# Performance work log

Hardware: AMD Instinct MI355X
Metric: run time of the kernel (lower is better)

Reference implementation:

```python
import jax, jax.numpy as jnp
import numpy as np

EMBED_DIM = 768
NUM_HEADS = 12
HEAD_DIM = EMBED_DIM // NUM_HEADS  # 64
SCALE = HEAD_DIM ** -0.5
B, S = 32, 512


def setup_inputs() -> dict:
    key = jax.random.key(0)
    ks = jax.random.split(key, 10)
    std = EMBED_DIM ** -0.5
    hidden_states = jax.random.normal(ks[0], (B, S, EMBED_DIM), dtype=jnp.float32)
    # causal mask: 0 on/below diagonal, large negative above
    neg = jnp.full((S, S), -1e9, dtype=jnp.float32)
    causal_attention_mask = jnp.broadcast_to(
        jnp.triu(neg, k=1)[None, None, :, :], (B, 1, S, S)
    ).astype(jnp.float32)
    Wq = jax.random.normal(ks[1], (EMBED_DIM, EMBED_DIM), dtype=jnp.float32) * std
    bq = jnp.zeros((EMBED_DIM,), dtype=jnp.float32)
    Wk = jax.random.normal(ks[2], (EMBED_DIM, EMBED_DIM), dtype=jnp.float32) * std
    bk = jnp.zeros((EMBED_DIM,), dtype=jnp.float32)
    Wv = jax.random.normal(ks[3], (EMBED_DIM, EMBED_DIM), dtype=jnp.float32) * std
    bv = jnp.zeros((EMBED_DIM,), dtype=jnp.float32)
    Wo = jax.random.normal(ks[4], (EMBED_DIM, EMBED_DIM), dtype=jnp.float32) * std
    bo = jnp.zeros((EMBED_DIM,), dtype=jnp.float32)
    return {
        "hidden_states": hidden_states,
        "causal_attention_mask": causal_attention_mask,
        "Wq": Wq, "bq": bq, "Wk": Wk, "bk": bk,
        "Wv": Wv, "bv": bv, "Wo": Wo, "bo": bo,
    }


def reference(hidden_states, causal_attention_mask, Wq, bq, Wk, bk, Wv, bv, Wo, bo):
    b, s, e = hidden_states.shape
    # projections; query scaled as in original
    q = (hidden_states @ Wq + bq) * SCALE          # [b,s,e]
    k = hidden_states @ Wk + bk
    v = hidden_states @ Wv + bv
    # [b,h,s,d]
    q = q.reshape(b, s, NUM_HEADS, HEAD_DIM).transpose(0, 2, 1, 3)
    k = k.reshape(b, s, NUM_HEADS, HEAD_DIM).transpose(0, 2, 1, 3)
    v = v.reshape(b, s, NUM_HEADS, HEAD_DIM).transpose(0, 2, 1, 3)
    scores = jnp.einsum("bhqd,bhkd->bhqk", q, k) + causal_attention_mask
    attn = jax.nn.softmax(scores, axis=-1)
    out = jnp.einsum("bhqk,bhkd->bhqd", attn, v)   # [b,h,s,d]
    out = out.transpose(0, 2, 1, 3).reshape(b, s, e)
    return out @ Wo + bo
```

## Files before the change

### kernel.cpp

```cpp
#include <hip/hip_runtime.h>
#include <hip/hip_bf16.h>

typedef __attribute__((ext_vector_type(8))) short bf16x8;
typedef __attribute__((ext_vector_type(4))) float f32x4;
typedef unsigned short u16;
typedef unsigned int u32;

#define MFMA16(a,b,c) __builtin_amdgcn_mfma_f32_16x16x32_bf16((a),(b),(c),0,0,0)
#define FENCE() asm volatile("" ::: "memory")
#define BARRIER() do { FENCE(); __builtin_amdgcn_s_barrier(); FENCE(); } while (0)
#define WAITV(N) asm volatile("s_waitcnt vmcnt(" #N ")" ::: "memory")

__device__ __forceinline__ u16 f2bf(float f) {
  union { float f; u32 u; } c; c.f = f;
  u32 u = c.u;
  return (u16)((u + 0x7FFFu + ((u >> 16) & 1u)) >> 16);
}

__device__ __forceinline__ u32 pk2(float lo, float hi) {
  __hip_bfloat162 h2 = __float22bfloat162_rn(float2{lo, hi});
  union { __hip_bfloat162 h; u32 u; } c; c.h = h2; return c.u;
}

__device__ __forceinline__ void gl_lds16(const u16* g, u16* l) {
  __builtin_amdgcn_global_load_lds((const __attribute__((address_space(1))) void*)g,
                                   (__attribute__((address_space(3))) void*)l, 16, 0, 0);
}

__global__ __launch_bounds__(256) void prep(const float* __restrict__ X,
                                            u16* __restrict__ Xb,
                                            const float* __restrict__ Wq,
                                            const float* __restrict__ Wk,
                                            const float* __restrict__ Wv,
                                            const float* __restrict__ Wo,
                                            u16* __restrict__ WT) {
  const int blk = blockIdx.x, tid = threadIdx.x;
  if (blk < 6144) {
    int i = (blk * 256 + tid) * 8;
    const float4* p = (const float4*)(X + i);
    float4 a = p[0], b = p[1];
    union { u16 h[8]; uint4 v; } o;
    o.h[0] = f2bf(a.x); o.h[1] = f2bf(a.y); o.h[2] = f2bf(a.z); o.h[3] = f2bf(a.w);
    o.h[4] = f2bf(b.x); o.h[5] = f2bf(b.y); o.h[6] = f2bf(b.z); o.h[7] = f2bf(b.w);
    *(uint4*)(Xb + i) = o.v;
  } else {
    __shared__ float t[32][33];
    const int q = blk - 6144;
    const int w = q / 576, p = q % 576;
    const float* W = (w == 0) ? Wq : (w == 1) ? Wk : (w == 2) ? Wv : Wo;
    u16* D = WT + (size_t)w * 768 * 768;
    const int n0 = (p % 24) * 32, k0 = (p / 24) * 32;
    const int tx = tid & 31, ty = tid >> 5;
#pragma unroll
    for (int i = 0; i < 4; ++i)
      t[ty + i * 8][tx] = W[(size_t)(k0 + ty + i * 8) * 768 + n0 + tx];
    __syncthreads();
#pragma unroll
    for (int i = 0; i < 4; ++i)
      D[(size_t)(n0 + ty + i * 8) * 768 + k0 + tx] = f2bf(t[tx][ty + i * 8]);
  }
}


#define STA2(bu, t, q) do { \
    const int r_ = (q) * 64 + (tid >> 3); \
    const int g_ = tid & 7; \
    gl_lds16(A + (size_t)(M0 + r_) * 768 + (t) * 64 + ((g_ ^ (r_ & 7)) << 3), \
             &As[bu][r_ * 64 + g_ * 8]); \
  } while (0)
#define STB3(bu, t, h) do { \
    const int r_ = (h) * 64 + (tid >> 3); \
    const int g_ = tid & 7; \
    gl_lds16(BT + (size_t)(N0 + r_) * 768 + (t) * 64 + ((g_ ^ (r_ & 7)) << 3), \
             &Bs[bu][r_ * 64 + g_ * 8]); \
  } while (0)

template <int MODE>
__global__ __launch_bounds__(512, 4)
void gemmR(const u16* __restrict__ A, const u16* __restrict__ BT,
           const float* __restrict__ b0, const float* __restrict__ b1,
           const float* __restrict__ b2,
           u16* __restrict__ oQ, u16* __restrict__ oK, u16* __restrict__ oV,
           float* __restrict__ oF, int nN) {
  constexpr int NT = 12;
  __shared__ __align__(16) u16 As[2][128 * 64];
  __shared__ __align__(16) u16 Bs[2][192 * 64];
  const int tid = threadIdx.x;
  const int wave = tid >> 6, lane = tid & 63;
  const int lg = lane >> 4, l15 = lane & 15;
  const int wr = wave >> 2, wc = wave & 3;
  const int bi = blockIdx.x;
  const int j = bi >> 3;
  const int M0 = ((bi & 7) * 16 + j / nN) * 128;
  const int N0 = (j % nN) * 192;

  f32x4 acc[4][3] = {};

  STA2(0, 0, 0); STA2(0, 0, 1);
  STB3(0, 0, 0); STB3(0, 0, 1); STB3(0, 0, 2);

#pragma unroll
  for (int t = 0; t < NT; ++t) {
    WAITV(0);
    BARRIER();
    if (t + 1 < NT) {
      const int nb = (t + 1) & 1;
      STA2(nb, t + 1, 0); STA2(nb, t + 1, 1);
      STB3(nb, t + 1, 0); STB3(nb, t + 1, 1); STB3(nb, t + 1, 2);
    }
    const int bb = t & 1;
    __builtin_amdgcn_s_setprio(1);
    bf16x8 bfr[3][2];
#pragma unroll
    for (int nt = 0; nt < 3; ++nt)
#pragma unroll
      for (int kh = 0; kh < 2; ++kh) {
        const int row = wc * 48 + nt * 16 + l15;
        bfr[nt][kh] = *(const bf16x8*)&Bs[bb][row * 64 + (((kh * 4 + lg) ^ (row & 7)) << 3)];
      }
#pragma unroll
    for (int mt = 0; mt < 4; ++mt) {
      bf16x8 af[2];
#pragma unroll
      for (int kh = 0; kh < 2; ++kh) {
        const int row = wr * 64 + mt * 16 + l15;
        af[kh] = *(const bf16x8*)&As[bb][row * 64 + (((kh * 4 + lg) ^ (row & 7)) << 3)];
      }
#pragma unroll
      for (int nt = 0; nt < 3; ++nt)
#pragma unroll
        for (int kh = 0; kh < 2; ++kh)
          acc[mt][nt] = MFMA16(af[kh], bfr[nt][kh], acc[mt][nt]);
    }
    __builtin_amdgcn_s_setprio(0);
  }

#pragma unroll
  for (int mt = 0; mt < 4; ++mt) {
    const int r0 = M0 + wr * 64 + mt * 16 + lg * 4;
#pragma unroll
    for (int nt = 0; nt < 3; ++nt) {
      const int ng = N0 + wc * 48 + nt * 16 + l15;
      f32x4 v = acc[mt][nt];
      if (MODE == 1) {
        const float bb = b0[ng];
#pragma unroll
        for (int r = 0; r < 4; ++r)
          oF[(size_t)(r0 + r) * 768 + ng] = v[r] + bb;
      } else {
        const int mat = ng / 768;
        const int col = ng - mat * 768;
        const float bb = (mat == 0 ? b0 : (mat == 1 ? b1 : b2))[col];
        if (mat == 0) {
#pragma unroll
          for (int r = 0; r < 4; ++r)
            oQ[(size_t)(r0 + r) * 768 + col] = f2bf((v[r] + bb) * 0.125f);
        } else if (mat == 1) {
#pragma unroll
          for (int r = 0; r < 4; ++r)
            oK[(size_t)(r0 + r) * 768 + col] = f2bf(v[r] + bb);
        } else {
          const int hh = col >> 6, dd = col & 63;
#pragma unroll
          for (int r = 0; r < 4; ++r) {
            const int rr = r0 + r;
            const int bbx = rr >> 9, ss = rr & 511;
            oV[((size_t)(bbx * 12 + hh) * 64 + dd) * 512 + ss] = f2bf(v[r] + bb);
          }
        }
      }
    }
  }
}

#define STG(bu, kt) do { \
    gl_lds16(Kg0 + (size_t)((kt) * 64 + srow) * 768 + sgr * 8, \
             &Ks[bu][srow * 64 + (tid & 7) * 8]); \
    gl_lds16(Vg0 + (size_t)srow * 512 + (kt) * 64 + sgr * 8, \
             &Vs[bu][srow * 64 + (tid & 7) * 8]); \
  } while (0)

__device__ __forceinline__ void attn_step(const u16* ks, const u16* vs, u32* pw,
                                          const bf16x8 qf[2], f32x4 oacc[4],
                                          float& m_run, float& l_run,
                                          int kt, int qbase, int lg, int l15) {
  if (kt * 64 > qbase + 15) return;
  f32x4 sc[4] = {};
#pragma unroll
  for (int kc = 0; kc < 2; ++kc)
#pragma unroll
    for (int t = 0; t < 4; ++t) {
      const int row = t * 16 + l15;
      bf16x8 kf = *(const bf16x8*)&ks[row * 64 + (((kc * 4 + lg) ^ (l15 & 7)) << 3)];
      sc[t] = MFMA16(kf, qf[kc], sc[t]);
    }
  if (kt * 64 + 63 > qbase) {
#pragma unroll
    for (int t = 0; t < 4; ++t)
#pragma unroll
      for (int r = 0; r < 4; ++r)
        if (kt * 64 + t * 16 + lg * 4 + r > qbase + l15) sc[t][r] = -1e30f;
  }
  float pm = sc[0][0];
#pragma unroll
  for (int t = 0; t < 4; ++t)
#pragma unroll
    for (int r = 0; r < 4; ++r) pm = fmaxf(pm, sc[t][r]);
  pm = fmaxf(pm, __shfl_xor(pm, 16));
  pm = fmaxf(pm, __shfl_xor(pm, 32));
  if (__any(pm > m_run + 8.f)) {
    const float mn = fmaxf(m_run, pm);
    const float fs = __expf(m_run - mn);
    m_run = mn;
    l_run *= fs;
#pragma unroll
    for (int t = 0; t < 4; ++t)
#pragma unroll
      for (int r = 0; r < 4; ++r) oacc[t][r] *= fs;
  }
  float rs = 0.f;
#pragma unroll
  for (int t = 0; t < 4; ++t) {
    float p0 = __expf(sc[t][0] - m_run), p1 = __expf(sc[t][1] - m_run);
    float p2 = __expf(sc[t][2] - m_run), p3 = __expf(sc[t][3] - m_run);
    rs += (p0 + p1) + (p2 + p3);
    pw[l15 * 36 + t * 8 + lg * 2 + 0] = pk2(p0, p1);
    pw[l15 * 36 + t * 8 + lg * 2 + 1] = pk2(p2, p3);
  }
  rs += __shfl_xor(rs, 16);
  rs += __shfl_xor(rs, 32);
  l_run += rs;
#pragma unroll
  for (int kc = 0; kc < 2; ++kc) {
    bf16x8 pf = *(const bf16x8*)&pw[l15 * 36 + kc * 16 + lg * 4];
#pragma unroll
    for (int t = 0; t < 4; ++t) {
      const int row = t * 16 + l15;
      bf16x8 vf = *(const bf16x8*)&vs[row * 64 + (((kc * 4 + lg) ^ (l15 & 7)) << 3)];
      oacc[t] = MFMA16(vf, pf, oacc[t]);
    }
  }
}

__global__ __launch_bounds__(512, 2)
void flash(const u16* __restrict__ Q, const u16* __restrict__ K,
           const u16* __restrict__ V, u16* __restrict__ O) {
  __shared__ __align__(16) u16 Ks[2][4096];
  __shared__ __align__(16) u16 Vs[2][4096];
  __shared__ __align__(16) u32 Ps[8][16 * 36];
  const int id = blockIdx.x;
  const int pair = id >> 9 >= 0 ? (id >= 384) : 0;
  const int hb = id - (pair ? 384 : 0);
  const int h = hb % 12, b = hb / 12;
  const int tid = threadIdx.x, wave = tid >> 6, lane = tid & 63;
  const int lg = lane >> 4, l15 = lane & 15;
  const int qA = pair ? 2 : 3;
  const int qB = pair ? 1 : 0;
  const int NT = 2 * qA + 2;
  const int srow = tid >> 3, sgr = (tid & 7) ^ (srow & 7);
  const int qbaseA = qA * 128 + wave * 16;
  const int qbaseB = qB * 128 + wave * 16;

  bf16x8 qfA[2], qfB[2];
  {
    const u16* qp = Q + (size_t)(b * 512 + qbaseA + l15) * 768 + h * 64 + lg * 8;
    qfA[0] = *(const bf16x8*)qp;
    qfA[1] = *(const bf16x8*)(qp + 32);
    const u16* qp2 = Q + (size_t)(b * 512 + qbaseB + l15) * 768 + h * 64 + lg * 8;
    qfB[0] = *(const bf16x8*)qp2;
    qfB[1] = *(const bf16x8*)(qp2 + 32);
  }
  f32x4 oaccA[4] = {}, oaccB[4] = {};
  float mA = -1e30f, lA = 0.f, mB = -1e30f, lB = 0.f;
  const u16* Kg0 = K + (size_t)(b * 512) * 768 + h * 64;
  const u16* Vg0 = V + (size_t)(b * 12 + h) * 64 * 512;
  u32* pw = Ps[wave];

  STG(0, 0);
  for (int kt = 0; kt < NT; ++kt) {
    WAITV(0);
    BARRIER();
    if (kt + 1 < NT) STG((kt + 1) & 1, kt + 1);
    const int bu = kt & 1;
    attn_step(Ks[bu], Vs[bu], pw, qfA, oaccA, mA, lA, kt, qbaseA, lg, l15);
    attn_step(Ks[bu], Vs[bu], pw, qfB, oaccB, mB, lB, kt, qbaseB, lg, l15);
  }
  {
    const float inv = 1.f / lA;
    u16* op = O + (size_t)(b * 512 + qbaseA + l15) * 768 + h * 64;
#pragma unroll
    for (int t = 0; t < 4; ++t) {
      uint2 w;
      w.x = pk2(oaccA[t][0] * inv, oaccA[t][1] * inv);
      w.y = pk2(oaccA[t][2] * inv, oaccA[t][3] * inv);
      *(uint2*)(op + t * 16 + lg * 4) = w;
    }
  }
  {
    const float inv = 1.f / lB;
    u16* op = O + (size_t)(b * 512 + qbaseB + l15) * 768 + h * 64;
#pragma unroll
    for (int t = 0; t < 4; ++t) {
      uint2 w;
      w.x = pk2(oaccB[t][0] * inv, oaccB[t][1] * inv);
      w.y = pk2(oaccB[t][2] * inv, oaccB[t][3] * inv);
      *(uint2*)(op + t * 16 + lg * 4) = w;
    }
  }
}

extern "C" void kernel_launch(void* const* d_in, const int* in_sizes, int n_in,
                              void* d_out, int out_size, void* d_ws, size_t ws_size,
                              hipStream_t stream) {
  (void)in_sizes; (void)n_in; (void)out_size; (void)ws_size;
  const float* X  = (const float*)d_in[0];
  const float* Wq = (const float*)d_in[2];
  const float* bq = (const float*)d_in[3];
  const float* Wk = (const float*)d_in[4];
  const float* bk = (const float*)d_in[5];
  const float* Wv = (const float*)d_in[6];
  const float* bv = (const float*)d_in[7];
  const float* Wo = (const float*)d_in[8];
  const float* bo = (const float*)d_in[9];
  float* out = (float*)d_out;

  const size_t NME = (size_t)16384 * 768;
  u16* Xb  = (u16*)d_ws;
  u16* Qs  = Xb + NME;
  u16* Kb  = Qs + NME;
  u16* Vt  = Kb + NME;
  u16* WT  = Vt + NME;
  u16* WoT = WT + (size_t)2304 * 768;
  u16* Ao  = Xb;

  prep<<<8448, 256, 0, stream>>>(X, Xb, Wq, Wk, Wv, Wo, WT);
  gemmR<0><<<1536, 512, 0, stream>>>(Xb, WT, bq, bk, bv, Qs, Kb, Vt, nullptr, 12);
  flash<<<768, 512, 0, stream>>>(Qs, Kb, Vt, Ao);
  gemmR<1><<<512, 512, 0, stream>>>(Ao, WoT, bo, nullptr, nullptr,
                                    nullptr, nullptr, nullptr, out, 4);
}
```

Before: 152.6 us.

## Enlarge GEMM tile to 256x192 with interleaved load/compute phases

The projection GEMMs now use 256-row M tiles, with each wave owning 128 rows. Each k-step is split into four sub-phases, and the global-to-LDS loads for the next buffer are interleaved between MFMA groups using partial vmcnt waits instead of one full wait per step. The goal is to hide load latency and reuse each B fragment across twice as many rows. In exchange, occupancy drops to 2 blocks per CU, the grid is halved, and there are many more barriers per iteration. There is also a small cleanup of the pair computation in the flash kernel.

New measurement: 157.6 us. 3.3% more time.

```diff
diff --git a/kernel.cpp b/kernel.cpp
--- a/kernel.cpp
+++ b/kernel.cpp
@@ -10,6 +10,8 @@
 #define FENCE() asm volatile("" ::: "memory")
 #define BARRIER() do { FENCE(); __builtin_amdgcn_s_barrier(); FENCE(); } while (0)
 #define WAITV(N) asm volatile("s_waitcnt vmcnt(" #N ")" ::: "memory")
+#define LG0() do { asm volatile("s_waitcnt lgkmcnt(0)" ::: "memory"); \
+                   __builtin_amdgcn_sched_barrier(0); } while (0)
 
 __device__ __forceinline__ u16 f2bf(float f) {
   union { float f; u32 u; } c; c.f = f;
@@ -62,28 +64,37 @@
 }
 
 
-#define STA2(bu, t, q) do { \
+#define GSTA(bu, t, q) do { \
     const int r_ = (q) * 64 + (tid >> 3); \
     const int g_ = tid & 7; \
     gl_lds16(A + (size_t)(M0 + r_) * 768 + (t) * 64 + ((g_ ^ (r_ & 7)) << 3), \
              &As[bu][r_ * 64 + g_ * 8]); \
   } while (0)
-#define STB3(bu, t, h) do { \
-    const int r_ = (h) * 64 + (tid >> 3); \
+#define GSTB(bu, t, q) do { \
+    const int r_ = (q) * 64 + (tid >> 3); \
     const int g_ = tid & 7; \
     gl_lds16(BT + (size_t)(N0 + r_) * 768 + (t) * 64 + ((g_ ^ (r_ & 7)) << 3), \
              &Bs[bu][r_ * 64 + g_ * 8]); \
   } while (0)
+#define RDA(bb, mh, kh) do { _Pragma("unroll") for (int mt_ = 0; mt_ < 4; ++mt_) { \
+    const int row_ = wr * 128 + (mh) * 64 + mt_ * 16 + l15; \
+    af[mt_] = *(const bf16x8*)&As[bb][row_ * 64 + ((((kh) * 4 + lg) ^ (row_ & 7)) << 3)]; } } while (0)
+#define RDB(bb, kh, dst) do { _Pragma("unroll") for (int nt_ = 0; nt_ < 3; ++nt_) { \
+    const int row_ = wc * 48 + nt_ * 16 + l15; \
+    dst[nt_] = *(const bf16x8*)&Bs[bb][row_ * 64 + ((((kh) * 4 + lg) ^ (row_ & 7)) << 3)]; } } while (0)
+#define MM12(mh, bfr) do { _Pragma("unroll") for (int mt_ = 0; mt_ < 4; ++mt_) \
+    _Pragma("unroll") for (int nt_ = 0; nt_ < 3; ++nt_) \
+      acc[(mh) * 4 + mt_][nt_] = MFMA16(af[mt_], bfr[nt_], acc[(mh) * 4 + mt_][nt_]); } while (0)
 
 template <int MODE>
-__global__ __launch_bounds__(512, 4)
-void gemmR(const u16* __restrict__ A, const u16* __restrict__ BT,
+__global__ __launch_bounds__(512, 2)
+void gemmT(const u16* __restrict__ A, const u16* __restrict__ BT,
            const float* __restrict__ b0, const float* __restrict__ b1,
            const float* __restrict__ b2,
            u16* __restrict__ oQ, u16* __restrict__ oK, u16* __restrict__ oV,
            float* __restrict__ oF, int nN) {
   constexpr int NT = 12;
-  __shared__ __align__(16) u16 As[2][128 * 64];
+  __shared__ __align__(16) u16 As[2][256 * 64];
   __shared__ __align__(16) u16 Bs[2][192 * 64];
   const int tid = threadIdx.x;
   const int wave = tid >> 6, lane = tid & 63;
@@ -91,57 +102,49 @@
   const int wr = wave >> 2, wc = wave & 3;
   const int bi = blockIdx.x;
   const int j = bi >> 3;
-  const int M0 = ((bi & 7) * 16 + j / nN) * 128;
+  const int M0 = ((bi & 7) * 8 + j / nN) * 256;
   const int N0 = (j % nN) * 192;
 
-  f32x4 acc[4][3] = {};
-
-  STA2(0, 0, 0); STA2(0, 0, 1);
-  STB3(0, 0, 0); STB3(0, 0, 1); STB3(0, 0, 2);
+  f32x4 acc[8][3] = {};
+  bf16x8 af[4], bfr0[3], bfr1[3];
+
+  GSTB(0, 0, 0); GSTB(0, 0, 1); GSTB(0, 0, 2);
+  GSTA(0, 0, 0); GSTA(0, 0, 2); GSTA(0, 0, 1); GSTA(0, 0, 3);
 
 #pragma unroll
   for (int t = 0; t < NT; ++t) {
-    WAITV(0);
-    BARRIER();
-    if (t + 1 < NT) {
-      const int nb = (t + 1) & 1;
-      STA2(nb, t + 1, 0); STA2(nb, t + 1, 1);
-      STB3(nb, t + 1, 0); STB3(nb, t + 1, 1); STB3(nb, t + 1, 2);
-    }
-    const int bb = t & 1;
-    __builtin_amdgcn_s_setprio(1);
-    bf16x8 bfr[3][2];
-#pragma unroll
-    for (int nt = 0; nt < 3; ++nt)
-#pragma unroll
-      for (int kh = 0; kh < 2; ++kh) {
-        const int row = wc * 48 + nt * 16 + l15;
-        bfr[nt][kh] = *(const bf16x8*)&Bs[bb][row * 64 + (((kh * 4 + lg) ^ (row & 7)) << 3)];
-      }
-#pragma unroll
-    for (int mt = 0; mt < 4; ++mt) {
-      bf16x8 af[2];
-#pragma unroll
-      for (int kh = 0; kh < 2; ++kh) {
-        const int row = wr * 64 + mt * 16 + l15;
-        af[kh] = *(const bf16x8*)&As[bb][row * 64 + (((kh * 4 + lg) ^ (row & 7)) << 3)];
-      }
-#pragma unroll
-      for (int nt = 0; nt < 3; ++nt)
-#pragma unroll
-        for (int kh = 0; kh < 2; ++kh)
-          acc[mt][nt] = MFMA16(af[kh], bfr[nt][kh], acc[mt][nt]);
-    }
-    __builtin_amdgcn_s_setprio(0);
-  }
-
-#pragma unroll
-  for (int mt = 0; mt < 4; ++mt) {
-    const int r0 = M0 + wr * 64 + mt * 16 + lg * 4;
-#pragma unroll
-    for (int nt = 0; nt < 3; ++nt) {
-      const int ng = N0 + wc * 48 + nt * 16 + l15;
-      f32x4 v = acc[mt][nt];
+    const int bb = t & 1, nb = bb ^ 1;
+    WAITV(2);
+    BARRIER();
+    RDA(bb, 0, 0); RDB(bb, 0, bfr0);
+    if (t + 1 < NT) { GSTB(nb, t + 1, 0); GSTB(nb, t + 1, 1); }
+    BARRIER(); LG0();
+    __builtin_amdgcn_s_setprio(1); MM12(0, bfr0); __builtin_amdgcn_s_setprio(0);
+    BARRIER();
+    RDA(bb, 0, 1); RDB(bb, 1, bfr1);
+    if (t + 1 < NT) { GSTB(nb, t + 1, 2); GSTA(nb, t + 1, 0); }
+    BARRIER(); LG0();
+    __builtin_amdgcn_s_setprio(1); MM12(0, bfr1); __builtin_amdgcn_s_setprio(0);
+    if (t + 1 < NT) { WAITV(4); } else { WAITV(0); }
+    BARRIER();
+    RDA(bb, 1, 0);
+    if (t + 1 < NT) { GSTA(nb, t + 1, 2); }
+    BARRIER(); LG0();
+    __builtin_amdgcn_s_setprio(1); MM12(1, bfr0); __builtin_amdgcn_s_setprio(0);
+    BARRIER();
+    RDA(bb, 1, 1);
+    if (t + 1 < NT) { GSTA(nb, t + 1, 1); GSTA(nb, t + 1, 3); }
+    BARRIER(); LG0();
+    __builtin_amdgcn_s_setprio(1); MM12(1, bfr1); __builtin_amdgcn_s_setprio(0);
+  }
+
+#pragma unroll
+  for (int mi = 0; mi < 8; ++mi) {
+    const int r0 = M0 + wr * 128 + mi * 16 + lg * 4;
+#pragma unroll
+    for (int ni = 0; ni < 3; ++ni) {
+      const int ng = N0 + wc * 48 + ni * 16 + l15;
+      f32x4 v = acc[mi][ni];
       if (MODE == 1) {
         const float bb = b0[ng];
 #pragma unroll
@@ -249,7 +252,7 @@
   __shared__ __align__(16) u16 Vs[2][4096];
   __shared__ __align__(16) u32 Ps[8][16 * 36];
   const int id = blockIdx.x;
-  const int pair = id >> 9 >= 0 ? (id >= 384) : 0;
+  const int pair = (id >= 384) ? 1 : 0;
   const int hb = id - (pair ? 384 : 0);
   const int h = hb % 12, b = hb / 12;
   const int tid = threadIdx.x, wave = tid >> 6, lane = tid & 63;
@@ -334,8 +337,8 @@
   u16* Ao  = Xb;
 
   prep<<<8448, 256, 0, stream>>>(X, Xb, Wq, Wk, Wv, Wo, WT);
-  gemmR<0><<<1536, 512, 0, stream>>>(Xb, WT, bq, bk, bv, Qs, Kb, Vt, nullptr, 12);
+  gemmT<0><<<768, 512, 0, stream>>>(Xb, WT, bq, bk, bv, Qs, Kb, Vt, nullptr, 12);
   flash<<<768, 512, 0, stream>>>(Qs, Kb, Vt, Ao);
-  gemmR<1><<<512, 512, 0, stream>>>(Ao, WoT, bo, nullptr, nullptr,
+  gemmT<1><<<256, 512, 0, stream>>>(Ao, WoT, bo, nullptr, nullptr,
                                     nullptr, nullptr, nullptr, out, 4);
 }
```
